# Performance work log

Hardware: AMD Instinct MI355X
Metric: run time of the kernel (lower is better)

## Reference

```python
import jax, jax.numpy as jnp
import numpy as np

N, E, G = 50000, 800000, 64
IN_DIM, HID, HEADS = 8, 64, 4
HC = HID * HEADS  # 256
EPS = 1e-5


def _gatv2(h, src, dst, ea, wl, bl, wr, br, we, att, bias):
    # h: [N, F_in]; ea: [E, 1]; att: [HEADS, HID]
    xl = (h @ wl + bl).reshape(N, HEADS, HID)        # source transform
    xr = (h @ wr + br).reshape(N, HEADS, HID)        # target transform
    ee = (ea @ we).reshape(E, HEADS, HID)            # edge embedding (no bias)
    m = xl[src] + xr[dst] + ee                       # [E, H, C]
    m = jax.nn.leaky_relu(m, 0.2)
    logits = jnp.einsum('ehc,hc->eh', m, att)        # [E, H]
    # softmax over incoming edges of each target node
    mx = jax.ops.segment_max(logits, dst, num_segments=N)
    ex = jnp.exp(logits - mx[dst])
    den = jax.ops.segment_sum(ex, dst, num_segments=N)
    alpha = ex / den[dst]                            # [E, H]
    out = jax.ops.segment_sum(xl[src] * alpha[..., None], dst, num_segments=N)
    return out.reshape(N, HC) + bias


def setup_inputs() -> dict:
    key = jax.random.key(0)
    ks = jax.random.split(key, 32)
    s = lambda fan: 1.0 / np.sqrt(fan)
    d = {}
    d['x'] = jax.random.normal(ks[0], (N, IN_DIM), jnp.float32)
    d['edge_attr'] = jax.random.normal(ks[1], (E, 1), jnp.float32)
    d['edge_index'] = jax.random.randint(ks[2], (2, E), 0, N, jnp.int64)
    d['batch'] = jnp.sort(jax.random.randint(ks[3], (N,), 0, G, jnp.int64))
    d['enc_w'] = jax.random.normal(ks[4], (IN_DIM, HID), jnp.float32) * s(IN_DIM)
    d['enc_b'] = jnp.zeros((HID,), jnp.float32)
    # gat1: in = HID
    d['g1_wl'] = jax.random.normal(ks[5], (HID, HC), jnp.float32) * s(HID)
    d['g1_bl'] = jnp.zeros((HC,), jnp.float32)
    d['g1_wr'] = jax.random.normal(ks[6], (HID, HC), jnp.float32) * s(HID)
    d['g1_br'] = jnp.zeros((HC,), jnp.float32)
    d['g1_we'] = jax.random.normal(ks[7], (1, HC), jnp.float32)
    d['g1_att'] = jax.random.normal(ks[8], (HEADS, HID), jnp.float32) * s(HID)
    d['g1_bias'] = jnp.zeros((HC,), jnp.float32)
    # gat2: in = HC
    d['g2_wl'] = jax.random.normal(ks[9], (HC, HC), jnp.float32) * s(HC)
    d['g2_bl'] = jnp.zeros((HC,), jnp.float32)
    d['g2_wr'] = jax.random.normal(ks[10], (HC, HC), jnp.float32) * s(HC)
    d['g2_br'] = jnp.zeros((HC,), jnp.float32)
    d['g2_we'] = jax.random.normal(ks[11], (1, HC), jnp.float32)
    d['g2_att'] = jax.random.normal(ks[12], (HEADS, HID), jnp.float32) * s(HID)
    d['g2_bias'] = jnp.zeros((HC,), jnp.float32)
    # post MLP + head
    d['p1_w'] = jax.random.normal(ks[13], (HC, 128), jnp.float32) * s(HC)
    d['p1_b'] = jnp.zeros((128,), jnp.float32)
    d['ln_g'] = jnp.ones((128,), jnp.float32)
    d['ln_b'] = jnp.zeros((128,), jnp.float32)
    d['p2_w'] = jax.random.normal(ks[14], (128, HID), jnp.float32) * s(128)
    d['p2_b'] = jnp.zeros((HID,), jnp.float32)
    d['head_w'] = jax.random.normal(ks[15], (HID, 1), jnp.float32) * s(HID)
    d['head_b'] = jnp.zeros((1,), jnp.float32)
    return d


def reference(x, edge_attr, edge_index, batch, enc_w, enc_b,
              g1_wl, g1_bl, g1_wr, g1_br, g1_we, g1_att, g1_bias,
              g2_wl, g2_bl, g2_wr, g2_br, g2_we, g2_att, g2_bias,
              p1_w, p1_b, ln_g, ln_b, p2_w, p2_b, head_w, head_b):
    src, dst = edge_index[0], edge_index[1]
    h = jax.nn.relu(x @ enc_w + enc_b)
    h = jax.nn.relu(_gatv2(h, src, dst, edge_attr, g1_wl, g1_bl, g1_wr, g1_br, g1_we, g1_att, g1_bias))
    h = jax.nn.relu(_gatv2(h, src, dst, edge_attr, g2_wl, g2_bl, g2_wr, g2_br, g2_we, g2_att, g2_bias))
    # global mean pool over graphs
    counts = jax.ops.segment_sum(jnp.ones((N,), h.dtype), batch, num_segments=G)
    g = jax.ops.segment_sum(h, batch, num_segments=G) / jnp.maximum(counts, 1.0)[:, None]
    # post MLP: Linear -> LayerNorm -> ReLU -> (dropout=eval noop) -> Linear -> ReLU
    z = g @ p1_w + p1_b
    mu = jnp.mean(z, axis=-1, keepdims=True)
    var = jnp.var(z, axis=-1, keepdims=True)
    z = (z - mu) * jax.lax.rsqrt(var + EPS) * ln_g + ln_b
    z = jax.nn.relu(z)
    z = jax.nn.relu(z @ p2_w + p2_b)
    return (z @ head_w + head_b)[:, 0]
```

## Files before the change

kernel.cpp:

```cpp
#include <hip/hip_runtime.h>
#include <hip/hip_bf16.h>
#include <math.h>

#define N_NODES 50000
#define N_EDGES 800000
#define N_GRAPHS 64
#define HCD 256
#define HIDD 64


__global__ void zero_i32(int* __restrict__ p, int n) {
  int i = blockIdx.x * blockDim.x + threadIdx.x;
  if (i < n) p[i] = 0;
}

__global__ void hist_kernel(const int* __restrict__ dst, int* __restrict__ counts, int ne) {
  int i = blockIdx.x * blockDim.x + threadIdx.x;
  if (i < ne) atomicAdd(&counts[dst[i]], 1);
}

__global__ __launch_bounds__(256) void scan1_kernel(const int* __restrict__ counts,
                                                    int* __restrict__ offs,
                                                    int* __restrict__ bsum, int n) {
  int t = threadIdx.x, lane = t & 63, w = t >> 6;
  int i = blockIdx.x * 256 + t;
  int v = (i < n) ? counts[i] : 0;
  int x = v;
  #pragma unroll
  for (int off = 1; off < 64; off <<= 1) {
    int tmp = __shfl_up(x, off);
    if (lane >= off) x += tmp;
  }
  __shared__ int wsum[4], woff[4];
  if (lane == 63) wsum[w] = x;
  __syncthreads();
  if (t == 0) {
    int s = 0;
    #pragma unroll
    for (int k = 0; k < 4; ++k) { woff[k] = s; s += wsum[k]; }
    bsum[blockIdx.x] = s;
  }
  __syncthreads();
  if (i < n) offs[i] = woff[w] + x - v;
}

__global__ __launch_bounds__(256) void scan2_kernel(int* __restrict__ bsum, int nblk) {
  int t = threadIdx.x, lane = t & 63, w = t >> 6;
  int v = (t < nblk) ? bsum[t] : 0;
  int x = v;
  #pragma unroll
  for (int off = 1; off < 64; off <<= 1) {
    int tmp = __shfl_up(x, off);
    if (lane >= off) x += tmp;
  }
  __shared__ int wsum[4], woff[4];
  if (lane == 63) wsum[w] = x;
  __syncthreads();
  if (t == 0) {
    int s = 0;
    #pragma unroll
    for (int k = 0; k < 4; ++k) { woff[k] = s; s += wsum[k]; }
  }
  __syncthreads();
  if (t < nblk) bsum[t] = woff[w] + x - v;
}

__global__ void scan3_kernel(int* __restrict__ offs, const int* __restrict__ bsum, int n) {
  int i = blockIdx.x * blockDim.x + threadIdx.x;
  if (i < n) offs[i] += bsum[i >> 8];
  else if (i == n) offs[n] = N_EDGES;
}

__global__ void copy_i32(const int* __restrict__ a, int* __restrict__ b, int n) {
  int i = blockIdx.x * blockDim.x + threadIdx.x;
  if (i < n) b[i] = a[i];
}

__global__ void scatter_kernel(const int* __restrict__ src, const int* __restrict__ dst,
                               const float* __restrict__ ea, int* __restrict__ cursor,
                               int* __restrict__ ssrc, float* __restrict__ sea, int ne) {
  int i = blockIdx.x * blockDim.x + threadIdx.x;
  if (i < ne) {
    int d = dst[i];
    int pos = atomicAdd(&cursor[d], 1);
    ssrc[pos] = src[i];
    sea[pos] = ea[i];
  }
}


__global__ void encoder_kernel(const float* __restrict__ x, const float* __restrict__ w,
                               const float* __restrict__ b, float* __restrict__ h0, int n_nodes) {
  int idx = blockIdx.x * blockDim.x + threadIdx.x;
  if (idx >= n_nodes * HIDD) return;
  int n = idx >> 6, c = idx & 63;
  float acc = b[c];
  #pragma unroll
  for (int k = 0; k < 8; ++k) acc += x[n * 8 + k] * w[k * 64 + c];
  h0[idx] = fmaxf(acc, 0.f);
}


template<int K>
__global__ __launch_bounds__(256) void transform_kernel(
    const float* __restrict__ h,
    const float* __restrict__ wl, const float* __restrict__ bl,
    const float* __restrict__ wr, const float* __restrict__ br,
    float* __restrict__ xl, float* __restrict__ xr, int n_nodes)
{
  constexpr int NT = 32;
  __shared__ float hs[NT * K];
  int n0 = blockIdx.x * NT;
  for (int idx4 = threadIdx.x; idx4 < NT * K / 4; idx4 += 256) {
    int i = idx4 / (K / 4), kq = idx4 - i * (K / 4);
    int n = n0 + i;
    float4 v = make_float4(0.f, 0.f, 0.f, 0.f);
    if (n < n_nodes) v = *(const float4*)&h[n * K + 4 * kq];
    *(float4*)&hs[i * K + 4 * kq] = v;
  }
  __syncthreads();
  const int cx = threadIdx.x & 63;
  const int ny = threadIdx.x >> 6;
  float accL[8][4];
  float accR[8][4];
  #pragma unroll
  for (int i = 0; i < 8; ++i)
    #pragma unroll
    for (int j = 0; j < 4; ++j) { accL[i][j] = 0.f; accR[i][j] = 0.f; }
  const float* hrow = &hs[(ny * 8) * K];
  for (int k4 = 0; k4 < K; k4 += 4) {
    float4 h4[8];
    #pragma unroll
    for (int i = 0; i < 8; ++i) h4[i] = *(const float4*)&hrow[i * K + k4];
    #pragma unroll
    for (int kk = 0; kk < 4; ++kk) {
      float4 wl4 = *(const float4*)&wl[(k4 + kk) * 256 + 4 * cx];
      float4 wr4 = *(const float4*)&wr[(k4 + kk) * 256 + 4 * cx];
      #pragma unroll
      for (int i = 0; i < 8; ++i) {
        float hv = (kk == 0) ? h4[i].x : (kk == 1) ? h4[i].y : (kk == 2) ? h4[i].z : h4[i].w;
        accL[i][0] = fmaf(hv, wl4.x, accL[i][0]); accL[i][1] = fmaf(hv, wl4.y, accL[i][1]);
        accL[i][2] = fmaf(hv, wl4.z, accL[i][2]); accL[i][3] = fmaf(hv, wl4.w, accL[i][3]);
        accR[i][0] = fmaf(hv, wr4.x, accR[i][0]); accR[i][1] = fmaf(hv, wr4.y, accR[i][1]);
        accR[i][2] = fmaf(hv, wr4.z, accR[i][2]); accR[i][3] = fmaf(hv, wr4.w, accR[i][3]);
      }
    }
  }
  float4 bl4 = *(const float4*)&bl[4 * cx];
  float4 br4 = *(const float4*)&br[4 * cx];
  #pragma unroll
  for (int i = 0; i < 8; ++i) {
    int n = n0 + ny * 8 + i;
    if (n < n_nodes) {
      float4 o;
      o.x = accL[i][0] + bl4.x; o.y = accL[i][1] + bl4.y;
      o.z = accL[i][2] + bl4.z; o.w = accL[i][3] + bl4.w;
      *(float4*)&xl[n * 256 + 4 * cx] = o;
      o.x = accR[i][0] + br4.x; o.y = accR[i][1] + br4.y;
      o.z = accR[i][2] + br4.z; o.w = accR[i][3] + br4.w;
      *(float4*)&xr[n * 256 + 4 * cx] = o;
    }
  }
}


__global__ __launch_bounds__(256) void gat_aggregate_kernel(
    const float* __restrict__ xl, const float* __restrict__ xr,
    const int* __restrict__ offs, const int* __restrict__ ssrc,
    const float* __restrict__ sea,
    const float* __restrict__ we, const float* __restrict__ att,
    const float* __restrict__ bias, float* __restrict__ out, int n_nodes)
{
  int n = blockIdx.x;
  if (n >= n_nodes) return;
  int t = threadIdx.x, lane = t & 63, wv = t >> 6;
  const float4 xr4 = *(const float4*)&xr[n * HCD + 4 * lane];
  const float4 we4 = *(const float4*)&we[4 * lane];
  const float4 at4 = *(const float4*)&att[4 * lane];
  int beg = offs[n], end = offs[n + 1];
  float runmax = -INFINITY, den = 0.f;
  float4 acc = make_float4(0.f, 0.f, 0.f, 0.f);
  for (int j = beg + wv; j < end; j += 4) {
    int s = ssrc[j];
    float eav = sea[j];
    float4 xlv = *(const float4*)&xl[s * HCD + 4 * lane];
    float4 m;
    m.x = xlv.x + fmaf(eav, we4.x, xr4.x);
    m.y = xlv.y + fmaf(eav, we4.y, xr4.y);
    m.z = xlv.z + fmaf(eav, we4.z, xr4.z);
    m.w = xlv.w + fmaf(eav, we4.w, xr4.w);
    m.x = (m.x > 0.f) ? m.x : 0.2f * m.x;
    m.y = (m.y > 0.f) ? m.y : 0.2f * m.y;
    m.z = (m.z > 0.f) ? m.z : 0.2f * m.z;
    m.w = (m.w > 0.f) ? m.w : 0.2f * m.w;
    float p = fmaf(m.w, at4.w, fmaf(m.z, at4.z, fmaf(m.y, at4.y, m.x * at4.x)));
    #pragma unroll
    for (int off = 1; off < 16; off <<= 1) p += __shfl_xor(p, off);
    float nm = fmaxf(runmax, p);
    float sc = __expf(runmax - nm);
    float wgt = __expf(p - nm);
    den = fmaf(den, sc, wgt);
    acc.x = fmaf(acc.x, sc, wgt * xlv.x);
    acc.y = fmaf(acc.y, sc, wgt * xlv.y);
    acc.z = fmaf(acc.z, sc, wgt * xlv.z);
    acc.w = fmaf(acc.w, sc, wgt * xlv.w);
    runmax = nm;
  }
  __shared__ float smax[4][64], sden[4][64];
  __shared__ float4 sacc[4][64];
  smax[wv][lane] = runmax; sden[wv][lane] = den; sacc[wv][lane] = acc;
  __syncthreads();
  if (wv == 0) {
    float m0 = smax[0][lane], m1 = smax[1][lane], m2 = smax[2][lane], m3 = smax[3][lane];
    float M = fmaxf(fmaxf(m0, m1), fmaxf(m2, m3));
    float4 a = make_float4(0.f, 0.f, 0.f, 0.f);
    if (M > -INFINITY) {
      float s0 = __expf(m0 - M), s1 = __expf(m1 - M), s2 = __expf(m2 - M), s3 = __expf(m3 - M);
      float d = sden[0][lane] * s0 + sden[1][lane] * s1 + sden[2][lane] * s2 + sden[3][lane] * s3;
      float4 a0 = sacc[0][lane], a1 = sacc[1][lane], a2 = sacc[2][lane], a3 = sacc[3][lane];
      a.x = a0.x * s0 + a1.x * s1 + a2.x * s2 + a3.x * s3;
      a.y = a0.y * s0 + a1.y * s1 + a2.y * s2 + a3.y * s3;
      a.z = a0.z * s0 + a1.z * s1 + a2.z * s2 + a3.z * s3;
      a.w = a0.w * s0 + a1.w * s1 + a2.w * s2 + a3.w * s3;
      float inv = 1.f / d;
      a.x *= inv; a.y *= inv; a.z *= inv; a.w *= inv;
    }
    float4 b4 = *(const float4*)&bias[4 * lane];
    float4 o;
    o.x = fmaxf(a.x + b4.x, 0.f);
    o.y = fmaxf(a.y + b4.y, 0.f);
    o.z = fmaxf(a.z + b4.z, 0.f);
    o.w = fmaxf(a.w + b4.w, 0.f);
    *(float4*)&out[n * HCD + 4 * lane] = o;
  }
}


__device__ __forceinline__ int lbound(const int* __restrict__ a, int n, int key) {
  int lo = 0, hi = n;
  while (lo < hi) { int mid = (lo + hi) >> 1; if (a[mid] < key) lo = mid + 1; else hi = mid; }
  return lo;
}

__global__ __launch_bounds__(256) void pool_kernel(const float* __restrict__ h,
                                                   const int* __restrict__ batch,
                                                   float* __restrict__ gmean) {
  int g = blockIdx.x;
  int t = threadIdx.x, lane = t & 63, wv = t >> 6;
  __shared__ int sb, se;
  if (t == 0) {
    sb = lbound(batch, N_NODES, g);
    se = lbound(batch, N_NODES, g + 1);
  }
  __syncthreads();
  int beg = sb, end = se;
  float4 acc = make_float4(0.f, 0.f, 0.f, 0.f);
  for (int n = beg + wv; n < end; n += 4) {
    float4 v = *(const float4*)&h[n * HCD + 4 * lane];
    acc.x += v.x; acc.y += v.y; acc.z += v.z; acc.w += v.w;
  }
  __shared__ float4 sacc[4][64];
  sacc[wv][lane] = acc;
  __syncthreads();
  if (wv == 0) {
    float4 a0 = sacc[0][lane], a1 = sacc[1][lane], a2 = sacc[2][lane], a3 = sacc[3][lane];
    float cnt = (float)((end - beg) > 1 ? (end - beg) : 1);
    float inv = 1.f / cnt;
    float4 o;
    o.x = (a0.x + a1.x + a2.x + a3.x) * inv;
    o.y = (a0.y + a1.y + a2.y + a3.y) * inv;
    o.z = (a0.z + a1.z + a2.z + a3.z) * inv;
    o.w = (a0.w + a1.w + a2.w + a3.w) * inv;
    *(float4*)&gmean[g * HCD + 4 * lane] = o;
  }
}


__global__ __launch_bounds__(128) void mlp_kernel(
    const float* __restrict__ gmean,
    const float* __restrict__ p1_w, const float* __restrict__ p1_b,
    const float* __restrict__ ln_g, const float* __restrict__ ln_b,
    const float* __restrict__ p2_w, const float* __restrict__ p2_b,
    const float* __restrict__ head_w, const float* __restrict__ head_b,
    float* __restrict__ out)
{
  int g = blockIdx.x, t = threadIdx.x;
  __shared__ float gv[256];
  __shared__ float zs[128];
  __shared__ float z2s[64];
  __shared__ float sums[2][2];
  gv[t] = gmean[g * 256 + t];
  gv[t + 128] = gmean[g * 256 + 128 + t];
  __syncthreads();
  float acc = p1_b[t];
  for (int k = 0; k < 256; ++k) acc += gv[k] * p1_w[k * 128 + t];
  float s1 = acc, s2 = acc * acc;
  #pragma unroll
  for (int off = 32; off >= 1; off >>= 1) {
    s1 += __shfl_xor(s1, off);
    s2 += __shfl_xor(s2, off);
  }
  int wid = t >> 6, lane = t & 63;
  if (lane == 0) { sums[wid][0] = s1; sums[wid][1] = s2; }
  __syncthreads();
  float S1 = sums[0][0] + sums[1][0];
  float S2 = sums[0][1] + sums[1][1];
  float mu = S1 * (1.f / 128.f);
  float var = S2 * (1.f / 128.f) - mu * mu;
  float rstd = rsqrtf(var + 1e-5f);
  float z = (acc - mu) * rstd * ln_g[t] + ln_b[t];
  zs[t] = fmaxf(z, 0.f);
  __syncthreads();
  if (t < 64) {
    float a2 = p2_b[t];
    for (int k = 0; k < 128; ++k) a2 += zs[k] * p2_w[k * 64 + t];
    z2s[t] = fmaxf(a2, 0.f);
  }
  __syncthreads();
  if (t < 64) {
    float p = z2s[t] * head_w[t];
    #pragma unroll
    for (int off = 32; off >= 1; off >>= 1) p += __shfl_xor(p, off);
    if (t == 0) out[g] = p + head_b[0];
  }
}


extern "C" void kernel_launch(void* const* d_in, const int* in_sizes, int n_in,
                              void* d_out, int out_size, void* d_ws, size_t ws_size,
                              hipStream_t stream) {
  const float* x       = (const float*)d_in[0];
  const float* ea      = (const float*)d_in[1];
  const int*   eidx    = (const int*)d_in[2];
  const int*   batch   = (const int*)d_in[3];
  const float* enc_w   = (const float*)d_in[4];
  const float* enc_b   = (const float*)d_in[5];
  const float* g1_wl   = (const float*)d_in[6];
  const float* g1_bl   = (const float*)d_in[7];
  const float* g1_wr   = (const float*)d_in[8];
  const float* g1_br   = (const float*)d_in[9];
  const float* g1_we   = (const float*)d_in[10];
  const float* g1_att  = (const float*)d_in[11];
  const float* g1_bias = (const float*)d_in[12];
  const float* g2_wl   = (const float*)d_in[13];
  const float* g2_bl   = (const float*)d_in[14];
  const float* g2_wr   = (const float*)d_in[15];
  const float* g2_br   = (const float*)d_in[16];
  const float* g2_we   = (const float*)d_in[17];
  const float* g2_att  = (const float*)d_in[18];
  const float* g2_bias = (const float*)d_in[19];
  const float* p1_w    = (const float*)d_in[20];
  const float* p1_b    = (const float*)d_in[21];
  const float* ln_g    = (const float*)d_in[22];
  const float* ln_b    = (const float*)d_in[23];
  const float* p2_w    = (const float*)d_in[24];
  const float* p2_b    = (const float*)d_in[25];
  const float* head_w  = (const float*)d_in[26];
  const float* head_b  = (const float*)d_in[27];

  const int* src = eidx;
  const int* dst = eidx + N_EDGES;

  char* wsp = (char*)d_ws;
  size_t off = 0;
  auto alloc = [&](size_t bytes) -> void* {
    void* p = wsp + off;
    off += (bytes + 255) & ~(size_t)255;
    return p;
  };
  float* h0     = (float*)alloc((size_t)N_NODES * 64 * 4);
  float* hA     = (float*)alloc((size_t)N_NODES * 256 * 4);
  float* xl     = (float*)alloc((size_t)N_NODES * 256 * 4);
  float* xr     = (float*)alloc((size_t)N_NODES * 256 * 4);
  int*   counts = (int*)alloc((size_t)N_NODES * 4);
  int*   offs   = (int*)alloc((size_t)(N_NODES + 1) * 4);
  int*   cursor = (int*)alloc((size_t)N_NODES * 4);
  int*   bsum   = (int*)alloc((size_t)256 * 4);
  int*   ssrc   = (int*)alloc((size_t)N_EDGES * 4);
  float* seaf   = (float*)alloc((size_t)N_EDGES * 4);
  float* gmean  = (float*)alloc((size_t)N_GRAPHS * 256 * 4);

  const int NBLK = (N_NODES + 255) / 256;

  zero_i32<<<NBLK, 256, 0, stream>>>(counts, N_NODES);
  hist_kernel<<<(N_EDGES + 255) / 256, 256, 0, stream>>>(dst, counts, N_EDGES);
  scan1_kernel<<<NBLK, 256, 0, stream>>>(counts, offs, bsum, N_NODES);
  scan2_kernel<<<1, 256, 0, stream>>>(bsum, NBLK);
  scan3_kernel<<<(N_NODES + 256) / 256, 256, 0, stream>>>(offs, bsum, N_NODES);
  copy_i32<<<NBLK, 256, 0, stream>>>(offs, cursor, N_NODES);
  scatter_kernel<<<(N_EDGES + 255) / 256, 256, 0, stream>>>(src, dst, ea, cursor, ssrc, seaf, N_EDGES);

  encoder_kernel<<<(N_NODES * 64 + 255) / 256, 256, 0, stream>>>(x, enc_w, enc_b, h0, N_NODES);

  transform_kernel<64><<<(N_NODES + 31) / 32, 256, 0, stream>>>(
      h0, g1_wl, g1_bl, g1_wr, g1_br, xl, xr, N_NODES);
  gat_aggregate_kernel<<<N_NODES, 256, 0, stream>>>(
      xl, xr, offs, ssrc, seaf, g1_we, g1_att, g1_bias, hA, N_NODES);

  transform_kernel<256><<<(N_NODES + 31) / 32, 256, 0, stream>>>(
      hA, g2_wl, g2_bl, g2_wr, g2_br, xl, xr, N_NODES);
  gat_aggregate_kernel<<<N_NODES, 256, 0, stream>>>(
      xl, xr, offs, ssrc, seaf, g2_we, g2_att, g2_bias, hA, N_NODES);

  pool_kernel<<<N_GRAPHS, 256, 0, stream>>>(hA, batch, gmean);
  mlp_kernel<<<N_GRAPHS, 128, 0, stream>>>(gmean, p1_w, p1_b, ln_g, ln_b,
                                           p2_w, p2_b, head_w, head_b, (float*)d_out);
}
```

Baseline: 767.9 us.

## Split transform across grid y, prefetch edge indices, fuse cursor copy into scan

The transform kernel now computes either the left or the right projection per block, selected by blockIdx.y. This halves accumulator registers and doubles the grid, at the cost of loading the node tile twice. The aggregate loop software-prefetches the next edge's source index and attribute so their loads overlap with the current edge's gather. The separate cursor copy kernel is folded into scan3, removing one launch.

```diff
diff --git a/kernel.cpp b/kernel.cpp
--- a/kernel.cpp
+++ b/kernel.cpp
@@ -65,15 +65,16 @@
   if (t < nblk) bsum[t] = woff[w] + x - v;
 }
 
-__global__ void scan3_kernel(int* __restrict__ offs, const int* __restrict__ bsum, int n) {
+__global__ void scan3_kernel(int* __restrict__ offs, const int* __restrict__ bsum,
+                             int* __restrict__ cursor, int n) {
   int i = blockIdx.x * blockDim.x + threadIdx.x;
-  if (i < n) offs[i] += bsum[i >> 8];
-  else if (i == n) offs[n] = N_EDGES;
-}
-
-__global__ void copy_i32(const int* __restrict__ a, int* __restrict__ b, int n) {
-  int i = blockIdx.x * blockDim.x + threadIdx.x;
-  if (i < n) b[i] = a[i];
+  if (i < n) {
+    int v = offs[i] + bsum[i >> 8];
+    offs[i] = v;
+    cursor[i] = v;
+  } else if (i == n) {
+    offs[n] = N_EDGES;
+  }
 }
 
 __global__ void scatter_kernel(const int* __restrict__ src, const int* __restrict__ dst,
@@ -111,6 +112,10 @@
   constexpr int NT = 32;
   __shared__ float hs[NT * K];
   int n0 = blockIdx.x * NT;
+  const float* __restrict__ w   = blockIdx.y ? wr : wl;
+  const float* __restrict__ bb  = blockIdx.y ? br : bl;
+  float* __restrict__ outp      = blockIdx.y ? xr : xl;
+
   for (int idx4 = threadIdx.x; idx4 < NT * K / 4; idx4 += 256) {
     int i = idx4 / (K / 4), kq = idx4 - i * (K / 4);
     int n = n0 + i;
@@ -119,46 +124,40 @@
     *(float4*)&hs[i * K + 4 * kq] = v;
   }
   __syncthreads();
+
   const int cx = threadIdx.x & 63;
   const int ny = threadIdx.x >> 6;
-  float accL[8][4];
-  float accR[8][4];
+  float acc[8][4];
   #pragma unroll
   for (int i = 0; i < 8; ++i)
     #pragma unroll
-    for (int j = 0; j < 4; ++j) { accL[i][j] = 0.f; accR[i][j] = 0.f; }
+    for (int j = 0; j < 4; ++j) acc[i][j] = 0.f;
+
   const float* hrow = &hs[(ny * 8) * K];
-  for (int k4 = 0; k4 < K; k4 += 4) {
-    float4 h4[8];
-    #pragma unroll
-    for (int i = 0; i < 8; ++i) h4[i] = *(const float4*)&hrow[i * K + k4];
-    #pragma unroll
-    for (int kk = 0; kk < 4; ++kk) {
-      float4 wl4 = *(const float4*)&wl[(k4 + kk) * 256 + 4 * cx];
-      float4 wr4 = *(const float4*)&wr[(k4 + kk) * 256 + 4 * cx];
-      #pragma unroll
-      for (int i = 0; i < 8; ++i) {
-        float hv = (kk == 0) ? h4[i].x : (kk == 1) ? h4[i].y : (kk == 2) ? h4[i].z : h4[i].w;
-        accL[i][0] = fmaf(hv, wl4.x, accL[i][0]); accL[i][1] = fmaf(hv, wl4.y, accL[i][1]);
-        accL[i][2] = fmaf(hv, wl4.z, accL[i][2]); accL[i][3] = fmaf(hv, wl4.w, accL[i][3]);
-        accR[i][0] = fmaf(hv, wr4.x, accR[i][0]); accR[i][1] = fmaf(hv, wr4.y, accR[i][1]);
-        accR[i][2] = fmaf(hv, wr4.z, accR[i][2]); accR[i][3] = fmaf(hv, wr4.w, accR[i][3]);
-      }
+  float4 wc = *(const float4*)&w[4 * cx];
+  for (int k = 0; k < K; ++k) {
+    float4 wn = wc;
+    if (k + 1 < K) wn = *(const float4*)&w[(k + 1) * 256 + 4 * cx];
+    #pragma unroll
+    for (int i = 0; i < 8; ++i) {
+      float hv = hrow[i * K + k];
+      acc[i][0] = fmaf(hv, wc.x, acc[i][0]);
+      acc[i][1] = fmaf(hv, wc.y, acc[i][1]);
+      acc[i][2] = fmaf(hv, wc.z, acc[i][2]);
+      acc[i][3] = fmaf(hv, wc.w, acc[i][3]);
     }
-  }
-  float4 bl4 = *(const float4*)&bl[4 * cx];
-  float4 br4 = *(const float4*)&br[4 * cx];
+    wc = wn;
+  }
+
+  float4 b4 = *(const float4*)&bb[4 * cx];
   #pragma unroll
   for (int i = 0; i < 8; ++i) {
     int n = n0 + ny * 8 + i;
     if (n < n_nodes) {
       float4 o;
-      o.x = accL[i][0] + bl4.x; o.y = accL[i][1] + bl4.y;
-      o.z = accL[i][2] + bl4.z; o.w = accL[i][3] + bl4.w;
-      *(float4*)&xl[n * 256 + 4 * cx] = o;
-      o.x = accR[i][0] + br4.x; o.y = accR[i][1] + br4.y;
-      o.z = accR[i][2] + br4.z; o.w = accR[i][3] + br4.w;
-      *(float4*)&xr[n * 256 + 4 * cx] = o;
+      o.x = acc[i][0] + b4.x; o.y = acc[i][1] + b4.y;
+      o.z = acc[i][2] + b4.z; o.w = acc[i][3] + b4.w;
+      *(float4*)&outp[n * 256 + 4 * cx] = o;
     }
   }
 }
@@ -180,9 +179,14 @@
   int beg = offs[n], end = offs[n + 1];
   float runmax = -INFINITY, den = 0.f;
   float4 acc = make_float4(0.f, 0.f, 0.f, 0.f);
-  for (int j = beg + wv; j < end; j += 4) {
-    int s = ssrc[j];
-    float eav = sea[j];
+
+  int j = beg + wv;
+  int s = (j < end) ? ssrc[j] : 0;
+  float eav = (j < end) ? sea[j] : 0.f;
+  while (j < end) {
+    int jn = j + 4;
+    int s2 = 0; float ea2 = 0.f;
+    if (jn < end) { s2 = ssrc[jn]; ea2 = sea[jn]; }
     float4 xlv = *(const float4*)&xl[s * HCD + 4 * lane];
     float4 m;
     m.x = xlv.x + fmaf(eav, we4.x, xr4.x);
@@ -205,7 +209,9 @@
     acc.z = fmaf(acc.z, sc, wgt * xlv.z);
     acc.w = fmaf(acc.w, sc, wgt * xlv.w);
     runmax = nm;
-  }
+    s = s2; eav = ea2; j = jn;
+  }
+
   __shared__ float smax[4][64], sden[4][64];
   __shared__ float4 sacc[4][64];
   smax[wv][lane] = runmax; sden[wv][lane] = den; sacc[wv][lane] = acc;
@@ -386,18 +392,19 @@
   hist_kernel<<<(N_EDGES + 255) / 256, 256, 0, stream>>>(dst, counts, N_EDGES);
   scan1_kernel<<<NBLK, 256, 0, stream>>>(counts, offs, bsum, N_NODES);
   scan2_kernel<<<1, 256, 0, stream>>>(bsum, NBLK);
-  scan3_kernel<<<(N_NODES + 256) / 256, 256, 0, stream>>>(offs, bsum, N_NODES);
-  copy_i32<<<NBLK, 256, 0, stream>>>(offs, cursor, N_NODES);
+  scan3_kernel<<<(N_NODES + 256) / 256, 256, 0, stream>>>(offs, bsum, cursor, N_NODES);
   scatter_kernel<<<(N_EDGES + 255) / 256, 256, 0, stream>>>(src, dst, ea, cursor, ssrc, seaf, N_EDGES);
 
   encoder_kernel<<<(N_NODES * 64 + 255) / 256, 256, 0, stream>>>(x, enc_w, enc_b, h0, N_NODES);
 
-  transform_kernel<64><<<(N_NODES + 31) / 32, 256, 0, stream>>>(
+  const dim3 tgrid((N_NODES + 31) / 32, 2);
+
+  transform_kernel<64><<<tgrid, 256, 0, stream>>>(
       h0, g1_wl, g1_bl, g1_wr, g1_br, xl, xr, N_NODES);
   gat_aggregate_kernel<<<N_NODES, 256, 0, stream>>>(
       xl, xr, offs, ssrc, seaf, g1_we, g1_att, g1_bias, hA, N_NODES);
 
-  transform_kernel<256><<<(N_NODES + 31) / 32, 256, 0, stream>>>(
+  transform_kernel<256><<<tgrid, 256, 0, stream>>>(
       hA, g2_wl, g2_bl, g2_wr, g2_br, xl, xr, N_NODES);
   gat_aggregate_kernel<<<N_NODES, 256, 0, stream>>>(
       xl, xr, offs, ssrc, seaf, g2_we, g2_att, g2_bias, hA, N_NODES);
```

Result: no change. 755.5 us (-1.6%).
